# Kernel tuning notes

Hardware: AMD Instinct MI355X
Metric: run time of the kernel (lower is better)

The kernel has to match this reference:

```python
import jax, jax.numpy as jnp
import numpy as np

N_NODES = 50000


def _spmm(edge_index, edge_vals, dense):
    """Sparse [N,N] @ dense [N,D] via gather + segment-sum.
    edge_index[0] = row (dst), edge_index[1] = col (src)."""
    dst, src = edge_index[0], edge_index[1]
    msgs = edge_vals[:, None] * dense[src]  # [E, D]
    return jax.ops.segment_sum(msgs, dst, num_segments=N_NODES)


def setup_inputs() -> dict:
    key = jax.random.key(0)
    ks = jax.random.split(key, 8)
    N, D_IN, D_OUT, E = N_NODES, 128, 128, 800000
    x = jax.random.normal(ks[0], (N, D_IN), dtype=jnp.float32)
    # glorot init for weights
    scale = jnp.sqrt(6.0 / (D_IN + D_OUT)).astype(jnp.float32)
    W0 = jax.random.uniform(ks[1], (D_IN, D_OUT), jnp.float32, -scale, scale)
    W1 = jax.random.uniform(ks[2], (D_IN, D_OUT), jnp.float32, -scale, scale)
    bias = jnp.zeros((D_OUT,), dtype=jnp.float32)
    edge_vals0 = jax.random.uniform(ks[3], (E,), dtype=jnp.float32)
    edge_vals1 = jax.random.uniform(ks[4], (E,), dtype=jnp.float32)
    edge_index0 = jax.random.randint(ks[5], (2, E), 0, N, dtype=jnp.int32)
    edge_index1 = jax.random.randint(ks[6], (2, E), 0, N, dtype=jnp.int32)
    return {"x": x, "W0": W0, "W1": W1, "bias": bias,
            "edge_vals0": edge_vals0, "edge_vals1": edge_vals1,
            "edge_index0": edge_index0, "edge_index1": edge_index1}


def reference(x, W0, W1, bias, edge_vals0, edge_vals1, edge_index0, edge_index1):
    # dropout with rate 0 == identity (self.dropout unset in source snippet)
    pre0 = x @ W0  # [N, D_out]
    pre1 = x @ W1
    out = _spmm(edge_index0, edge_vals0, pre0) + _spmm(edge_index1, edge_vals1, pre1)
    out = out + bias
    return jax.nn.relu(out)
```

## Files before the change

### kernel.cpp

```cpp
#include <hip/hip_runtime.h>
#include <hip/hip_bf16.h>


#define BROWS 32
#define NBUCK 1563
#define NB2 2048
#define BCAP 704
#define ACAP (2 * BCAP)
#define FT6 4096
#define PREROWS 65536

typedef __attribute__((ext_vector_type(8))) short bf16x8;
typedef __attribute__((ext_vector_type(4))) float f32x4;

__device__ inline unsigned short f2bf(float f) {
    union { float f; unsigned u; } v; v.f = f;
    unsigned r = v.u + 0x7fff + ((v.u >> 16) & 1);
    return (unsigned short)(r >> 16);
}

__global__ __launch_bounds__(256) void prep_kernel(
    const float* __restrict__ W0, const float* __restrict__ W1,
    unsigned short* __restrict__ wt0, unsigned short* __restrict__ wt1,
    int* __restrict__ cur, int ncur)
{
    const int bid = blockIdx.x;
    const int tid = threadIdx.x;
    if (bid >= 8) {
        for (int i = tid; i < ncur; i += 256) cur[i] = 0;
        return;
    }
    const int which = bid >> 2;
    const int k0 = (bid & 3) * 32;
    const float* __restrict__ W = which ? W1 : W0;
    unsigned short* __restrict__ wt = which ? wt1 : wt0;
    for (int i = tid; i < 32 * 128; i += 256) {
        int k = k0 + (i >> 7), n = i & 127;
        wt[n * 128 + k] = f2bf(W[k * 128 + n]);
    }
}

__global__ __launch_bounds__(512) void gemm_fused_kernel(
    const float* __restrict__ x,
    const unsigned short* __restrict__ wt0,
    const unsigned short* __restrict__ wt1,
    unsigned short* __restrict__ pre,
    int N)
{
    __shared__ unsigned short sA[16][136];
    __shared__ short ctile[8][16][40];

    const int tid = threadIdx.x;
    const int m0 = blockIdx.x * 16;

    {
        int r = tid >> 5;
        int c4 = (tid & 31) << 2;
        float4 v = *(const float4*)&x[(m0 + r) * 128 + c4];
        ushort4 s;
        s.x = f2bf(v.x); s.y = f2bf(v.y); s.z = f2bf(v.z); s.w = f2bf(v.w);
        *(ushort4*)&sA[r][c4] = s;
    }
    __syncthreads();

    const int w = tid >> 6;
    const int lane = tid & 63;
    const int adj = w >> 2;
    const int wq = w & 3;
    const unsigned short* __restrict__ wt = adj ? wt1 : wt0;
    unsigned short* __restrict__ po = pre + (size_t)adj * PREROWS * 128;
    const int l15 = lane & 15;
    const int quad = lane >> 4;
    const int nA = wq * 32 + l15;

    f32x4 c0 = {0.f, 0.f, 0.f, 0.f};
    f32x4 c1 = {0.f, 0.f, 0.f, 0.f};
#pragma unroll
    for (int k0 = 0; k0 < 128; k0 += 32) {
        union { bf16x8 v; ushort4 h[2]; } au;
        au.h[0] = *(const ushort4*)&sA[l15][k0 + quad * 8];
        au.h[1] = *(const ushort4*)&sA[l15][k0 + quad * 8 + 4];
        bf16x8 b0 = *(const bf16x8*)&wt[nA * 128 + k0 + quad * 8];
        bf16x8 b1 = *(const bf16x8*)&wt[(nA + 16) * 128 + k0 + quad * 8];
        c0 = __builtin_amdgcn_mfma_f32_16x16x32_bf16(au.v, b0, c0, 0, 0, 0);
        c1 = __builtin_amdgcn_mfma_f32_16x16x32_bf16(au.v, b1, c1, 0, 0, 0);
    }

#pragma unroll
    for (int i = 0; i < 4; ++i) {
        ctile[w][quad * 4 + i][l15]      = (short)f2bf(c0[i]);
        ctile[w][quad * 4 + i][16 + l15] = (short)f2bf(c1[i]);
    }
    const int rr = lane >> 2, cg = (lane & 3) * 8;
    ushort4 s0 = *(ushort4*)&ctile[w][rr][cg];
    ushort4 s1 = *(ushort4*)&ctile[w][rr][cg + 4];
    int row = m0 + rr;
    *(ushort4*)&po[row * 128 + wq * 32 + cg] = s0;
    *(ushort4*)&po[row * 128 + wq * 32 + cg + 4] = s1;
}

__global__ __launch_bounds__(512) void fill6_kernel(
    const int* __restrict__ ei0, const int* __restrict__ ei1,
    const float* __restrict__ ev0, const float* __restrict__ ev1,
    int* __restrict__ cur, int2* __restrict__ recs, int E)
{
    __shared__ int2 srt[FT6];
    __shared__ alignas(16) int lcnt[NB2];
    __shared__ alignas(16) int lcur[NB2];
    __shared__ unsigned short skey[FT6];
    __shared__ int gpos[NBUCK];
    __shared__ int glim[NBUCK];
    __shared__ int wsum[8];
    __shared__ int stotal;

    const int tid = threadIdx.x;
    const int a = blockIdx.y;
    const int e0 = blockIdx.x * FT6;
    const int* __restrict__ ei = a ? ei1 : ei0;
    const float* __restrict__ ev = a ? ev1 : ev0;

    ((int4*)lcnt)[tid] = make_int4(0, 0, 0, 0);
    __syncthreads();

    const int eb = e0 + tid * 8;
    int dd[8], ss[8]; float vv[8];
    if (e0 + FT6 <= E) {
        int4 d0 = *(const int4*)(ei + eb);
        int4 d1 = *(const int4*)(ei + eb + 4);
        int4 s0 = *(const int4*)(ei + E + eb);
        int4 s1 = *(const int4*)(ei + E + eb + 4);
        float4 v0 = *(const float4*)(ev + eb);
        float4 v1 = *(const float4*)(ev + eb + 4);
        dd[0] = d0.x; dd[1] = d0.y; dd[2] = d0.z; dd[3] = d0.w;
        dd[4] = d1.x; dd[5] = d1.y; dd[6] = d1.z; dd[7] = d1.w;
        ss[0] = s0.x; ss[1] = s0.y; ss[2] = s0.z; ss[3] = s0.w;
        ss[4] = s1.x; ss[5] = s1.y; ss[6] = s1.z; ss[7] = s1.w;
        vv[0] = v0.x; vv[1] = v0.y; vv[2] = v0.z; vv[3] = v0.w;
        vv[4] = v1.x; vv[5] = v1.y; vv[6] = v1.z; vv[7] = v1.w;
    } else {
#pragma unroll
        for (int j = 0; j < 8; ++j) {
            int e = eb + j;
            if (e < E) { dd[j] = ei[e]; ss[j] = ei[E + e]; vv[j] = ev[e]; }
        }
    }
    int key8[8]; int2 rec[8];
#pragma unroll
    for (int j = 0; j < 8; ++j) {
        if (eb + j < E) {
            key8[j] = dd[j] >> 5;
            rec[j] = make_int2(((dd[j] & 31) << 17) | (a << 16) | ss[j],
                               __float_as_int(vv[j]));
            atomicAdd(&lcnt[key8[j]], 1);
        } else key8[j] = -1;
    }
    __syncthreads();

    const int lane = tid & 63;
    const int wv = tid >> 6;
    int4 c4 = ((const int4*)lcnt)[tid];
    int cc[4] = { c4.x, c4.y, c4.z, c4.w };
    int tsum = cc[0] + cc[1] + cc[2] + cc[3];
    int p = tsum;
#pragma unroll
    for (int o = 1; o < 64; o <<= 1) {
        int t = __shfl_up(p, o);
        if (lane >= o) p += t;
    }
    if (lane == 63) wsum[wv] = p;
    __syncthreads();
    int wbase = 0;
#pragma unroll
    for (int w2 = 0; w2 < 7; ++w2) wbase += (w2 < wv) ? wsum[w2] : 0;
    if (tid == 511) stotal = wbase + p;
    int off = wbase + p - tsum;
    const int k0 = 4 * tid;
#pragma unroll
    for (int h = 0; h < 4; ++h) {
        lcur[k0 + h] = off;
        if (k0 + h < NBUCK && cc[h] > 0) {
            int bin = (k0 + h) * 2 + a;
            int g = atomicAdd(&cur[bin], cc[h]);
            int lim = BCAP - g; if (lim < 0) lim = 0;
            gpos[k0 + h] = bin * BCAP + g;
            glim[k0 + h] = lim;
        }
        off += cc[h];
    }
    __syncthreads();

#pragma unroll
    for (int j = 0; j < 8; ++j) {
        if (key8[j] >= 0) {
            int pp = atomicAdd(&lcur[key8[j]], 1);
            srt[pp] = rec[j];
            skey[pp] = (unsigned short)key8[j];
        }
    }
    __syncthreads();

    const int total = stotal;
    for (int i = tid; i < total; i += 512) {
        int k = skey[i];
        int st = k ? lcur[k - 1] : 0;
        int r = i - st;
        if (r < glim[k]) recs[gpos[k] + r] = srt[i];
    }
}

__global__ __launch_bounds__(256, 8) void aggregate10_kernel(
    const int* __restrict__ cur, const int2* __restrict__ recs,
    const unsigned short* __restrict__ pre,
    const float* __restrict__ bias,
    float* __restrict__ out, int N)
{
    __shared__ int2 srt[ACAP];
    __shared__ int lcnt[32];
    __shared__ int lstart[32];
    __shared__ int lcur[32];

    const int b = blockIdx.x;
    const int tid = threadIdx.x;

    int n0 = cur[2 * b];     if (n0 > BCAP) n0 = BCAP;
    int n1 = cur[2 * b + 1]; if (n1 > BCAP) n1 = BCAP;
    const int total = n0 + n1;
    const int base0 = (2 * b) * BCAP, base1 = (2 * b + 1) * BCAP;

    if (tid < 32) lcnt[tid] = 0;
    __syncthreads();

    for (int i = tid; i < total; i += 256) {
        int2 r = (i < n0) ? recs[base0 + i] : recs[base1 + i - n0];
        atomicAdd(&lcnt[(r.x >> 17) & 31], 1);
    }
    __syncthreads();

    if (tid < 32) {
        int cme = lcnt[tid];
        int p = cme;
#pragma unroll
        for (int o = 1; o < 32; o <<= 1) {
            int t = __shfl_up(p, o);
            if (tid >= o) p += t;
        }
        lstart[tid] = p - cme;
        lcur[tid] = p - cme;
    }
    __syncthreads();

    for (int i = tid; i < total; i += 256) {
        int2 r = (i < n0) ? recs[base0 + i] : recs[base1 + i - n0];
        srt[atomicAdd(&lcur[(r.x >> 17) & 31], 1)] = r;
    }
    __syncthreads();

    const int wv = tid >> 6;
    const int lane = tid & 63;
    const float2 bi = *(const float2*)&bias[lane * 2];

#define GA(r) (*(const unsigned*)&pre[((r).x & 0x1ffff) * 128 + 2 * lane])
#define ACC(r, u) { float v = __int_as_float((r).y);                    \
        acc.x = fmaf(v, __uint_as_float((u) << 16), acc.x);             \
        acc.y = fmaf(v, __uint_as_float((u) & 0xffff0000u), acc.y); }

    for (int t = 0; t < 8; ++t) {
        const int rl = wv * 8 + t;
        const int s = lstart[rl];
        const int e = s + lcnt[rl];
        float2 acc = make_float2(0.f, 0.f);
        int j = s;
        for (; j + 8 <= e; j += 8) {
            int2 r0 = srt[j], r1 = srt[j + 1], r2 = srt[j + 2], r3 = srt[j + 3];
            int2 r4 = srt[j + 4], r5 = srt[j + 5], r6 = srt[j + 6], r7 = srt[j + 7];
            unsigned u0 = GA(r0), u1 = GA(r1), u2 = GA(r2), u3 = GA(r3);
            unsigned u4 = GA(r4), u5 = GA(r5), u6 = GA(r6), u7 = GA(r7);
            ACC(r0, u0); ACC(r1, u1); ACC(r2, u2); ACC(r3, u3);
            ACC(r4, u4); ACC(r5, u5); ACC(r6, u6); ACC(r7, u7);
        }
        for (; j + 4 <= e; j += 4) {
            int2 r0 = srt[j], r1 = srt[j + 1], r2 = srt[j + 2], r3 = srt[j + 3];
            unsigned u0 = GA(r0), u1 = GA(r1), u2 = GA(r2), u3 = GA(r3);
            ACC(r0, u0); ACC(r1, u1); ACC(r2, u2); ACC(r3, u3);
        }
        for (; j < e; ++j) {
            int2 r0 = srt[j];
            unsigned u0 = GA(r0);
            ACC(r0, u0);
        }
        int row = b * BROWS + rl;
        if (row < N) {
            float2 o;
            o.x = fmaxf(acc.x + bi.x, 0.f);
            o.y = fmaxf(acc.y + bi.y, 0.f);
            *(float2*)&out[row * 128 + 2 * lane] = o;
        }
    }
#undef GA
#undef ACC
}

extern "C" void kernel_launch(void* const* d_in, const int* in_sizes, int n_in,
                              void* d_out, int out_size, void* d_ws, size_t ws_size,
                              hipStream_t stream) {
    const float* x    = (const float*)d_in[0];
    const float* W0   = (const float*)d_in[1];
    const float* W1   = (const float*)d_in[2];
    const float* bias = (const float*)d_in[3];
    const float* ev0  = (const float*)d_in[4];
    const float* ev1  = (const float*)d_in[5];
    const int*   ei0  = (const int*)d_in[6];
    const int*   ei1  = (const int*)d_in[7];
    float* out = (float*)d_out;

    const int N = in_sizes[0] / 128;
    const int E = in_sizes[4];
    const int NBINS2 = NBUCK * 2;

    char* w = (char*)d_ws;
    unsigned short* pre = (unsigned short*)w;   w += (size_t)2 * PREROWS * 128 * 2;
    unsigned short* wt0 = (unsigned short*)w;   w += (size_t)128 * 128 * 2;
    unsigned short* wt1 = (unsigned short*)w;   w += (size_t)128 * 128 * 2;
    int* cur = (int*)w;                         w += (size_t)NBINS2 * 4;
    int2* recs = (int2*)w;                      w += (size_t)NBINS2 * BCAP * 8;

    prep_kernel<<<9, 256, 0, stream>>>(W0, W1, wt0, wt1, cur, NBINS2);

    gemm_fused_kernel<<<N / 16, 512, 0, stream>>>(x, wt0, wt1, pre, N);

    dim3 fgrid((E + FT6 - 1) / FT6, 2);
    fill6_kernel<<<fgrid, 512, 0, stream>>>(ei0, ei1, ev0, ev1, cur, recs, E);

    aggregate10_kernel<<<NBUCK, 256, 0, stream>>>(cur, recs, pre, bias, out, N);
}
```

Baseline: 226.2 us.

## Enlarge GEMM tile to 64 rows with register-resident weights; stage records in LDS

```diff
diff --git a/kernel.cpp b/kernel.cpp
--- a/kernel.cpp
+++ b/kernel.cpp
@@ -40,28 +40,31 @@
     }
 }
 
-__global__ __launch_bounds__(512) void gemm_fused_kernel(
+__global__ __launch_bounds__(512) void gemm64_kernel(
     const float* __restrict__ x,
     const unsigned short* __restrict__ wt0,
     const unsigned short* __restrict__ wt1,
     unsigned short* __restrict__ pre,
     int N)
 {
-    __shared__ unsigned short sA[16][136];
+    __shared__ unsigned short sA[64][136];
     __shared__ short ctile[8][16][40];
 
     const int tid = threadIdx.x;
-    const int m0 = blockIdx.x * 16;
-
-    {
-        int r = tid >> 5;
-        int c4 = (tid & 31) << 2;
-        float4 v = *(const float4*)&x[(m0 + r) * 128 + c4];
-        ushort4 s;
-        s.x = f2bf(v.x); s.y = f2bf(v.y); s.z = f2bf(v.z); s.w = f2bf(v.w);
-        *(ushort4*)&sA[r][c4] = s;
-    }
-    __syncthreads();
+    const int m0 = blockIdx.x * 64;
+
+#pragma unroll
+    for (int t = 0; t < 4; ++t) {
+        int idx = t * 512 + tid;
+        int r = idx >> 5;
+        int c4 = (idx & 31) << 2;
+        if (m0 + r < N) {
+            float4 v = *(const float4*)&x[(size_t)(m0 + r) * 128 + c4];
+            ushort4 s;
+            s.x = f2bf(v.x); s.y = f2bf(v.y); s.z = f2bf(v.z); s.w = f2bf(v.w);
+            *(ushort4*)&sA[r][c4] = s;
+        }
+    }
 
     const int w = tid >> 6;
     const int lane = tid & 63;
@@ -73,30 +76,38 @@
     const int quad = lane >> 4;
     const int nA = wq * 32 + l15;
 
-    f32x4 c0 = {0.f, 0.f, 0.f, 0.f};
-    f32x4 c1 = {0.f, 0.f, 0.f, 0.f};
-#pragma unroll
-    for (int k0 = 0; k0 < 128; k0 += 32) {
-        union { bf16x8 v; ushort4 h[2]; } au;
-        au.h[0] = *(const ushort4*)&sA[l15][k0 + quad * 8];
-        au.h[1] = *(const ushort4*)&sA[l15][k0 + quad * 8 + 4];
-        bf16x8 b0 = *(const bf16x8*)&wt[nA * 128 + k0 + quad * 8];
-        bf16x8 b1 = *(const bf16x8*)&wt[(nA + 16) * 128 + k0 + quad * 8];
-        c0 = __builtin_amdgcn_mfma_f32_16x16x32_bf16(au.v, b0, c0, 0, 0, 0);
-        c1 = __builtin_amdgcn_mfma_f32_16x16x32_bf16(au.v, b1, c1, 0, 0, 0);
-    }
-
-#pragma unroll
-    for (int i = 0; i < 4; ++i) {
-        ctile[w][quad * 4 + i][l15]      = (short)f2bf(c0[i]);
-        ctile[w][quad * 4 + i][16 + l15] = (short)f2bf(c1[i]);
-    }
+    bf16x8 b0[4], b1[4];
+#pragma unroll
+    for (int kk = 0; kk < 4; ++kk) {
+        b0[kk] = *(const bf16x8*)&wt[nA * 128 + kk * 32 + quad * 8];
+        b1[kk] = *(const bf16x8*)&wt[(nA + 16) * 128 + kk * 32 + quad * 8];
+    }
+    __syncthreads();
+
     const int rr = lane >> 2, cg = (lane & 3) * 8;
-    ushort4 s0 = *(ushort4*)&ctile[w][rr][cg];
-    ushort4 s1 = *(ushort4*)&ctile[w][rr][cg + 4];
-    int row = m0 + rr;
-    *(ushort4*)&po[row * 128 + wq * 32 + cg] = s0;
-    *(ushort4*)&po[row * 128 + wq * 32 + cg + 4] = s1;
+#pragma unroll
+    for (int mt = 0; mt < 4; ++mt) {
+        f32x4 c0 = {0.f, 0.f, 0.f, 0.f};
+        f32x4 c1 = {0.f, 0.f, 0.f, 0.f};
+#pragma unroll
+        for (int kk = 0; kk < 4; ++kk) {
+            union { bf16x8 v; ushort4 h[2]; } au;
+            au.h[0] = *(const ushort4*)&sA[mt * 16 + l15][kk * 32 + quad * 8];
+            au.h[1] = *(const ushort4*)&sA[mt * 16 + l15][kk * 32 + quad * 8 + 4];
+            c0 = __builtin_amdgcn_mfma_f32_16x16x32_bf16(au.v, b0[kk], c0, 0, 0, 0);
+            c1 = __builtin_amdgcn_mfma_f32_16x16x32_bf16(au.v, b1[kk], c1, 0, 0, 0);
+        }
+#pragma unroll
+        for (int i = 0; i < 4; ++i) {
+            ctile[w][quad * 4 + i][l15]      = (short)f2bf(c0[i]);
+            ctile[w][quad * 4 + i][16 + l15] = (short)f2bf(c1[i]);
+        }
+        int row = m0 + mt * 16 + rr;
+        if (row < N) {
+            int4 sv = *(const int4*)&ctile[w][rr][cg];
+            *(int4*)&po[(size_t)row * 128 + wq * 32 + cg] = sv;
+        }
+    }
 }
 
 __global__ __launch_bounds__(512) void fill6_kernel(
@@ -208,12 +219,13 @@
     }
 }
 
-__global__ __launch_bounds__(256, 8) void aggregate10_kernel(
+__global__ __launch_bounds__(256, 6) void aggregate9_kernel(
     const int* __restrict__ cur, const int2* __restrict__ recs,
     const unsigned short* __restrict__ pre,
     const float* __restrict__ bias,
     float* __restrict__ out, int N)
 {
+    __shared__ int2 srec[ACAP];
     __shared__ int2 srt[ACAP];
     __shared__ int lcnt[32];
     __shared__ int lstart[32];
@@ -232,6 +244,7 @@
 
     for (int i = tid; i < total; i += 256) {
         int2 r = (i < n0) ? recs[base0 + i] : recs[base1 + i - n0];
+        srec[i] = r;
         atomicAdd(&lcnt[(r.x >> 17) & 31], 1);
     }
     __syncthreads();
@@ -250,7 +263,7 @@
     __syncthreads();
 
     for (int i = tid; i < total; i += 256) {
-        int2 r = (i < n0) ? recs[base0 + i] : recs[base1 + i - n0];
+        int2 r = srec[i];
         srt[atomicAdd(&lcur[(r.x >> 17) & 31], 1)] = r;
     }
     __syncthreads();
@@ -326,10 +339,10 @@
 
     prep_kernel<<<9, 256, 0, stream>>>(W0, W1, wt0, wt1, cur, NBINS2);
 
-    gemm_fused_kernel<<<N / 16, 512, 0, stream>>>(x, wt0, wt1, pre, N);
+    gemm64_kernel<<<(N + 63) / 64, 512, 0, stream>>>(x, wt0, wt1, pre, N);
 
     dim3 fgrid((E + FT6 - 1) / FT6, 2);
     fill6_kernel<<<fgrid, 512, 0, stream>>>(ei0, ei1, ev0, ev1, cur, recs, E);
 
-    aggregate10_kernel<<<NBUCK, 256, 0, stream>>>(cur, recs, pre, bias, out, N);
-}
+    aggregate9_kernel<<<NBUCK, 256, 0, stream>>>(cur, recs, pre, bias, out, N);
+}
```

Result: faster. 210.7 us (-6.9%).
